# Optimization experiments

Measured on AMD Instinct MI355X. Metric: run time of the kernel, lower is better.

Reference implementation:

```python
import jax, jax.numpy as jnp
import numpy as np

LN_EPS = 1e-12
CHEB_K = 3
HIDDEN = 64


def _layernorm(x, w, b):
    m = jnp.mean(x, axis=-1, keepdims=True)
    v = jnp.mean((x - m) ** 2, axis=-1, keepdims=True)
    return (x - m) / jnp.sqrt(v + LN_EPS) * w + b


def _magcn(x, node_emb, time_emb, ln_w, ln_b, W_pool, b_pool):
    # x: [B,N,C]; node_emb: [N,D]; W_pool: [D,K,C,O]; b_pool: [D,O]
    e = _layernorm(node_emb + time_emb[None, :], ln_w, ln_b)  # dropout = identity (eval)
    supports = jax.nn.softmax(e @ e.T, axis=1)                # [N,N]
    N = e.shape[0]
    Ts = [jnp.eye(N, dtype=x.dtype), supports]
    for _ in range(2, CHEB_K):
        Ts.append(2.0 * supports @ Ts[-1] - Ts[-2])
    S = jnp.stack(Ts, axis=0)                                 # [K,N,N]
    weights = jnp.einsum('nd,dkio->nkio', e, W_pool)          # [N,K,C,O]
    bias = e @ b_pool                                         # [N,O]
    x_g = jnp.einsum('knm,bmc->bnkc', S, x)                   # [B,N,K,C]
    return jnp.einsum('bnki,nkio->bno', x_g, weights) + bias  # [B,N,O]


def setup_inputs() -> dict:
    key = jax.random.key(0)
    ks = jax.random.split(key, 10)
    B, N, C, H, D = 64, 1024, 64, HIDDEN, 16
    return {
        'x': jax.random.normal(ks[0], (B, N, C), jnp.float32),
        'norm_dis_matrix': jax.random.uniform(ks[1], (N, N), jnp.float32),
        'state': jax.random.normal(ks[2], (B, N, H), jnp.float32),
        'node_embeddings': jax.random.normal(ks[3], (N, D), jnp.float32),
        'node_flows': jax.random.normal(ks[4], (B, N), jnp.float32),
        'time_embeddings': jax.random.normal(ks[5], (D,), jnp.float32),
        'gate_W': jax.random.normal(ks[6], (D, CHEB_K, C + H, 2 * H), jnp.float32) * 0.1,
        'gate_b': jax.random.normal(ks[7], (D, 2 * H), jnp.float32) * 0.1,
        'gate_ln_w': jnp.ones((D,), jnp.float32),
        'gate_ln_b': jnp.zeros((D,), jnp.float32),
        'update_W': jax.random.normal(ks[8], (D, CHEB_K, C + H, H), jnp.float32) * 0.1,
        'update_b': jax.random.normal(ks[9], (D, H), jnp.float32) * 0.1,
        'update_ln_w': jnp.ones((D,), jnp.float32),
        'update_ln_b': jnp.zeros((D,), jnp.float32),
    }


def reference(x, norm_dis_matrix, state, node_embeddings, node_flows, time_embeddings,
              gate_W, gate_b, gate_ln_w, gate_ln_b,
              update_W, update_b, update_ln_w, update_ln_b):
    inp_state = jnp.concatenate([x, state], axis=-1)  # [B,N,C+H]
    z_r = jax.nn.sigmoid(_magcn(inp_state, node_embeddings, time_embeddings,
                                gate_ln_w, gate_ln_b, gate_W, gate_b))
    z, r = z_r[..., :HIDDEN], z_r[..., HIDDEN:]
    candidate = jnp.concatenate([x, z * state], axis=-1)
    hc = jnp.tanh(_magcn(candidate, node_embeddings, time_embeddings,
                         update_ln_w, update_ln_b, update_W, update_b))
    return r * state + (1.0 - r) * hc
```

## Files before the change

kernel.cpp:

```cpp
#include <hip/hip_runtime.h>
#include <hip/hip_bf16.h>

typedef __hip_bfloat16 bf16;
typedef __attribute__((ext_vector_type(8))) short bf16x8;
typedef __attribute__((ext_vector_type(4))) float f32x4;

constexpr int Bn = 64;
constexpr int Nn = 1024;
constexpr int Dd = 16;
constexpr int Cc = 64;
constexpr int Hh = 64;
constexpr int CI = 128;
constexpr int OG = 128;
constexpr int OU = 64;
constexpr int Jt = Bn * CI;

__device__ __forceinline__ float b2f(bf16 v) { return __bfloat162float(v); }
__device__ __forceinline__ float lo2f(unsigned u) { return __uint_as_float(u << 16); }
__device__ __forceinline__ float hi2f(unsigned u) { return __uint_as_float(u & 0xffff0000u); }
__device__ __forceinline__ float bfbits2f(unsigned short u) { return __uint_as_float(((unsigned)u) << 16); }
__device__ __forceinline__ unsigned short f2bfbits(float x) {
    bf16 h = __float2bfloat16(x);
    return *reinterpret_cast<unsigned short*>(&h);
}
__device__ __forceinline__ float rfl(float x) {
    return __int_as_float(__builtin_amdgcn_readfirstlane(__float_as_int(x)));
}

__device__ __forceinline__ float ldin(const void* p, size_t i, int flag) {
    return flag ? b2f(((const bf16*)p)[i]) : ((const float*)p)[i];
}

__device__ __forceinline__ void gload_lds16(const void* g, void* l) {
    __builtin_amdgcn_global_load_lds((const __attribute__((address_space(1))) void*)g,
                                     (__attribute__((address_space(3))) void*)l, 16, 0, 0);
}

__global__ void detect_kernel(const void* glnw, int* flag) {
    unsigned u = *(const unsigned*)glnw;
    *flag = (u == 0x3F800000u) ? 0 : 1;
}

__global__ void conv_f32(const void* __restrict__ src, float* __restrict__ dst,
                         int n, const int* __restrict__ flag) {
    const int f = *flag;
    for (int i = blockIdx.x * blockDim.x + threadIdx.x; i < n; i += gridDim.x * blockDim.x)
        dst[i] = ldin(src, i, f);
}

__global__ __launch_bounds__(256) void wtrans(const void* __restrict__ src, unsigned short* __restrict__ Wt,
                                              int O, int osh, const int* __restrict__ flag) {
    const int f = *flag;
    const int k0 = blockIdx.x * 64;
    const int d = blockIdx.y;
    __shared__ unsigned short tile[64][136];
    const int t = threadIdx.x;
    for (int idx = t; idx < 64 * O; idx += 256) {
        const int kk = idx >> osh, o = idx & (O - 1);
        tile[kk][o] = f2bfbits(ldin(src, ((size_t)d * 384 + k0 + kk) * O + o, f));
    }
    __syncthreads();
    for (int idx = t; idx < O * 64; idx += 256) {
        const int o = idx >> 6, kk = idx & 63;
        Wt[((size_t)d * O + o) * 384 + k0 + kk] = tile[kk][o];
    }
}

__global__ void ln_kernel(const void* __restrict__ nemb, const void* __restrict__ temb,
                          const void* __restrict__ wg, const void* __restrict__ bg,
                          const void* __restrict__ wu, const void* __restrict__ bu,
                          float* __restrict__ e_g, float* __restrict__ e_u,
                          const int* __restrict__ flag) {
    const int f = *flag;
    int t = blockIdx.x * blockDim.x + threadIdx.x;
    if (t >= 2 * Nn) return;
    int which = t >> 10;
    int n = t & (Nn - 1);
    float v[Dd];
    float mean = 0.f;
#pragma unroll
    for (int d = 0; d < Dd; d++) { v[d] = ldin(nemb, n * Dd + d, f) + ldin(temb, d, f); mean += v[d]; }
    mean *= (1.f / Dd);
    float var = 0.f;
#pragma unroll
    for (int d = 0; d < Dd; d++) { float c = v[d] - mean; var += c * c; }
    var *= (1.f / Dd);
    float inv = 1.f / sqrtf(var + 1e-12f);
    const void* w = which ? wu : wg;
    const void* bb = which ? bu : bg;
    float* e = which ? e_u : e_g;
#pragma unroll
    for (int d = 0; d < Dd; d++)
        e[n * Dd + d] = (v[d] - mean) * inv * ldin(w, d, f) + ldin(bb, d, f);
}

__global__ __launch_bounds__(256) void attn_kernel(const float* __restrict__ e, bf16* __restrict__ A) {
    __shared__ float en[Dd];
    __shared__ float logits[Nn];
    __shared__ float red[256];
    const int n = blockIdx.x, t = threadIdx.x;
    if (t < Dd) en[t] = e[n * Dd + t];
    __syncthreads();
    float lmax = -1e30f;
    for (int m = t; m < Nn; m += 256) {
        float s = 0.f;
#pragma unroll
        for (int d = 0; d < Dd; d++) s += en[d] * e[m * Dd + d];
        logits[m] = s;
        lmax = fmaxf(lmax, s);
    }
    red[t] = lmax; __syncthreads();
    for (int s = 128; s > 0; s >>= 1) { if (t < s) red[t] = fmaxf(red[t], red[t + s]); __syncthreads(); }
    const float M = red[0];
    __syncthreads();
    float lsum = 0.f;
    for (int m = t; m < Nn; m += 256) { float p = expf(logits[m] - M); logits[m] = p; lsum += p; }
    red[t] = lsum; __syncthreads();
    for (int s = 128; s > 0; s >>= 1) { if (t < s) red[t] += red[t + s]; __syncthreads(); }
    const float inv = 1.f / red[0];
    for (int m = t; m < Nn; m += 256) A[(size_t)n * Nn + m] = __float2bfloat16(logits[m] * inv);
}

__global__ __launch_bounds__(256) void build_xg0(const void* __restrict__ x, const void* __restrict__ oth,
                                                 bf16* __restrict__ xg0t, bf16* __restrict__ xg0s,
                                                 const int* __restrict__ flag, int oth_bf16) {
    const int f = *flag;
    const int b = blockIdx.x;
    const int n0 = blockIdx.y * 64;
    __shared__ bf16 tile[128][68];
    const int t = threadIdx.x;
#pragma unroll
    for (int idx = t; idx < 64 * 128; idx += 256) {
        const int n = idx >> 7, i = idx & 127;
        const size_t base = ((size_t)b << 10) + n0 + n;
        float v;
        if (i < Cc) v = ldin(x, base * Cc + i, f);
        else v = oth_bf16 ? b2f(((const bf16*)oth)[base * Hh + i - Cc])
                          : ldin(oth, base * Hh + i - Cc, f);
        tile[i][n] = __float2bfloat16(v);
        xg0s[base * CI + i] = tile[i][n];
    }
    __syncthreads();
#pragma unroll
    for (int idx = t; idx < 128 * 64; idx += 256) {
        const int i = idx >> 6, n = idx & 63;
        xg0t[((size_t)(b * CI + i) << 10) + n0 + n] = tile[i][n];
    }
}

__global__ __launch_bounds__(256) void agg_mfma(const bf16* __restrict__ Amat,
                                                const bf16* __restrict__ Xmat,
                                                const bf16* __restrict__ Sub,
                                                bf16* __restrict__ Ct,
                                                bf16* __restrict__ Cs,
                                                int cheb, int write_t) {
    __shared__ bf16 Atile[128 * 32];
    __shared__ bf16 Xtile[128 * 32];
    __shared__ unsigned short Ts[128 * 136];
    char* AtileC = (char*)Atile;
    char* XtileC = (char*)Xtile;

    const int t = threadIdx.x;
    const int lane = t & 63, w = t >> 6;
    const int j0 = blockIdx.x * 128;
    const int m0 = blockIdx.y * 128;
    const int wr = (w >> 1) * 64, wc = (w & 1) * 64;
    const int lr = lane & 15, lq = lane >> 4;

    f32x4 acc[4][4];
#pragma unroll
    for (int a = 0; a < 4; a++)
#pragma unroll
        for (int b = 0; b < 4; b++) acc[a][b] = (f32x4){0.f, 0.f, 0.f, 0.f};

    const int srow = w * 16 + (lane >> 2);
    const int scb = (lane & 3) * 16;

    for (int k0 = 0; k0 < Nn; k0 += 32) {
        __syncthreads();
#pragma unroll
        for (int p = 0; p < 2; p++) {
            const int row = p * 64 + srow;
            gload_lds16((const char*)Amat + (size_t)(m0 + row) * 2048 + k0 * 2 + scb,
                        AtileC + p * 4096 + w * 1024);
            gload_lds16((const char*)Xmat + (size_t)(j0 + row) * 2048 + k0 * 2 + scb,
                        XtileC + p * 4096 + w * 1024);
        }
        __syncthreads();
        bf16x8 af[4], xf[4];
#pragma unroll
        for (int fr = 0; fr < 4; fr++)
            af[fr] = *(const bf16x8*)(AtileC + (wr + fr * 16 + lr) * 64 + lq * 16);
#pragma unroll
        for (int fc = 0; fc < 4; fc++)
            xf[fc] = *(const bf16x8*)(XtileC + (wc + fc * 16 + lr) * 64 + lq * 16);
#pragma unroll
        for (int fr = 0; fr < 4; fr++)
#pragma unroll
            for (int fc = 0; fc < 4; fc++)
                acc[fr][fc] = __builtin_amdgcn_mfma_f32_16x16x32_bf16(af[fr], xf[fc], acc[fr][fc], 0, 0, 0);
    }

#pragma unroll
    for (int fr = 0; fr < 4; fr++) {
        const int ml = wr + fr * 16 + lq * 4;
        const int m = m0 + ml;
#pragma unroll
        for (int fc = 0; fc < 4; fc++) {
            const int i = wc + fc * 16 + lr;
            const int j = j0 + i;
            f32x4 v = acc[fr][fc];
            const size_t off = ((size_t)j << 10) + m;
            if (cheb) {
                const ushort4 s = *(const ushort4*)((const unsigned short*)Sub + off);
                v.x = 2.f * v.x - bfbits2f(s.x);
                v.y = 2.f * v.y - bfbits2f(s.y);
                v.z = 2.f * v.z - bfbits2f(s.z);
                v.w = 2.f * v.w - bfbits2f(s.w);
            }
            ushort4 o4;
            o4.x = f2bfbits(v.x); o4.y = f2bfbits(v.y); o4.z = f2bfbits(v.z); o4.w = f2bfbits(v.w);
            if (write_t) *(ushort4*)((unsigned short*)Ct + off) = o4;
            const unsigned short* pv = (const unsigned short*)&o4;
#pragma unroll
            for (int q = 0; q < 4; q++) Ts[(ml + q) * 136 + i] = pv[q];
        }
    }
    __syncthreads();
    const int b = j0 >> 7;
#pragma unroll
    for (int p = 0; p < 8; p++) {
        const int u = p * 256 + t;
        const int m = u >> 4, ig = (u & 15) * 8;
        const uint4 val = *(const uint4*)&Ts[m * 136 + ig];
        *(uint4*)((unsigned short*)Cs + (((size_t)b << 10) + m0 + m) * 128 + ig) = val;
    }
}

template<int G, int GATE>
__global__ __launch_bounds__(256, 2) void pernode_gemm(
    const bf16* __restrict__ x0, const bf16* __restrict__ x1, const bf16* __restrict__ x2,
    const float* __restrict__ e, const unsigned short* __restrict__ Wt,
    const float* __restrict__ bpool,
    const void* __restrict__ state, const float* __restrict__ r_in,
    bf16* __restrict__ zs, float* __restrict__ r_out, void* __restrict__ out,
    const int* __restrict__ flag)
{
    constexpr int OSTR = GATE ? 128 : 64;
    const int f = *flag;
    const int bx = blockIdx.x;
    const int grp = GATE ? (bx >> 1) : bx;
    const int obase = GATE ? ((bx & 1) << 6) : 0;
    const int n0 = grp * G;

    __shared__ bf16 Wl[8 * 64 * 32];
    __shared__ bf16 Xl[G * 64 * 32];
    char* WlC = (char*)Wl;
    char* XlC = (char*)Xl;

    const int t = threadIdx.x;
    const int lane = t & 63, w = t >> 6;
    const int lr = lane & 15, lq = lane >> 4;
    const int og = obase + w * 16 + lr;

    float en[G][16];
#pragma unroll
    for (int nl = 0; nl < G; nl++)
#pragma unroll
        for (int d = 0; d < 16; d++) en[nl][d] = rfl(e[(n0 + nl) * 16 + d]);

    f32x4 acc[G][4];
#pragma unroll
    for (int nl = 0; nl < G; nl++)
#pragma unroll
        for (int mt = 0; mt < 4; mt++) acc[nl][mt] = (f32x4){0.f, 0.f, 0.f, 0.f};

    const bf16* xs[3] = {x0, x1, x2};

#pragma unroll 1
    for (int ch = 0; ch < 3; ch++) {
        const bf16* Xsrc = xs[ch];
#pragma unroll 1
        for (int ks = 0; ks < 4; ks++) {
            float wacc[G][8];
#pragma unroll
            for (int nl = 0; nl < G; nl++)
#pragma unroll
                for (int j = 0; j < 8; j++) wacc[nl][j] = 0.f;

#pragma unroll
            for (int dh = 0; dh < 2; dh++) {
                __syncthreads();
#pragma unroll
                for (int p = 0; p < 8; p++) {
                    const int u = p * 256 + w * 64 + lane;
                    const int r = u >> 2, kg = u & 3;
                    const int d = r >> 6, ol = r & 63;
                    gload_lds16(Wt + ((size_t)((dh * 8 + d) * OSTR + obase + ol) * 384)
                                   + ch * 128 + ks * 32 + kg * 8,
                                WlC + u * 16);
                }
                if (dh == 0) {
#pragma unroll
                    for (int p = 0; p < G; p++) {
                        const int u = p * 256 + w * 64 + lane;
                        const int r = u >> 2, kg = u & 3;
                        const int nl = r >> 6, b = r & 63;
                        gload_lds16(Xsrc + (((size_t)b << 10) + n0 + nl) * 128 + ks * 32 + kg * 8,
                                    XlC + u * 16);
                    }
                }
                __syncthreads();
#pragma unroll
                for (int d = 0; d < 8; d++) {
                    const bf16x8 wv = *(const bf16x8*)(WlC + (d * 64 + w * 16 + lr) * 64 + lq * 16);
                    const unsigned* wu = (const unsigned*)&wv;
                    float v[8];
                    v[0] = lo2f(wu[0]); v[1] = hi2f(wu[0]);
                    v[2] = lo2f(wu[1]); v[3] = hi2f(wu[1]);
                    v[4] = lo2f(wu[2]); v[5] = hi2f(wu[2]);
                    v[6] = lo2f(wu[3]); v[7] = hi2f(wu[3]);
#pragma unroll
                    for (int nl = 0; nl < G; nl++) {
                        const float ed = en[nl][dh * 8 + d];
#pragma unroll
                        for (int j = 0; j < 8; j++) wacc[nl][j] += ed * v[j];
                    }
                }
            }
#pragma unroll
            for (int nl = 0; nl < G; nl++) {
                union U8 { bf16x8 v; unsigned short s[8]; } bh, bl;
#pragma unroll
                for (int j = 0; j < 8; j++) {
                    const unsigned short h = f2bfbits(wacc[nl][j]);
                    bh.s[j] = h;
                    bl.s[j] = f2bfbits(wacc[nl][j] - bfbits2f(h));
                }
#pragma unroll
                for (int mt = 0; mt < 4; mt++) {
                    const bf16x8 af = *(const bf16x8*)(XlC + (nl * 64 + mt * 16 + lr) * 64 + lq * 16);
                    acc[nl][mt] = __builtin_amdgcn_mfma_f32_16x16x32_bf16(af, bh.v, acc[nl][mt], 0, 0, 0);
                    acc[nl][mt] = __builtin_amdgcn_mfma_f32_16x16x32_bf16(af, bl.v, acc[nl][mt], 0, 0, 0);
                }
            }
        }
    }

    const int ol = og & 63;
#pragma unroll
    for (int nl = 0; nl < G; nl++) {
        const int n_ = n0 + nl;
        float bias = 0.f;
#pragma unroll
        for (int d = 0; d < 16; d++) bias += en[nl][d] * bpool[d * OSTR + og];
#pragma unroll
        for (int mt = 0; mt < 4; mt++) {
            const f32x4 a = acc[nl][mt];
#pragma unroll
            for (int q = 0; q < 4; q++) {
                const int b = mt * 16 + lq * 4 + q;
                const size_t idx = (((size_t)b << 10) + n_) * 64 + ol;
                const float v = a[q] + bias;
                if (GATE) {
                    const float sg = 1.f / (1.f + expf(-v));
                    if (obase == 0) {
                        const float st = ldin(state, idx, f);
                        zs[idx] = __float2bfloat16(sg * st);
                    } else {
                        r_out[idx] = sg;
                    }
                } else {
                    const float hc = tanhf(v);
                    const float r = r_in[idx];
                    const float st = ldin(state, idx, f);
                    const float o = r * st + (1.f - r) * hc;
                    if (f) ((bf16*)out)[idx] = __float2bfloat16(o);
                    else   ((float*)out)[idx] = o;
                }
            }
        }
    }
}

extern "C" void kernel_launch(void* const* d_in, const int* in_sizes, int n_in,
                              void* d_out, int out_size, void* d_ws, size_t ws_size,
                              hipStream_t stream) {
    const void* x     = d_in[0];
    const void* state = d_in[2];
    const void* nemb  = d_in[3];
    const void* temb  = d_in[5];
    const void* gW    = d_in[6];
    const void* gb    = d_in[7];
    const void* glnw  = d_in[8];
    const void* glnb  = d_in[9];
    const void* uW    = d_in[10];
    const void* ub    = d_in[11];
    const void* ulnw  = d_in[12];
    const void* ulnb  = d_in[13];

    constexpr int GW_N = Dd * 3 * CI * OG;
    constexpr int GB_N = Dd * OG;
    constexpr int UW_N = Dd * 3 * CI * OU;
    constexpr int UB_N = Dd * OU;

    char* base = (char*)d_ws;
    size_t off = 0;
    auto carve = [&](size_t bytes) { char* p = base + off; off += (bytes + 255) & ~(size_t)255; return p; };
    int*   flag = (int*)carve(4);
    unsigned short* gWt = (unsigned short*)carve(GW_N * 2);
    unsigned short* uWt = (unsigned short*)carve(UW_N * 2);
    float* gbf = (float*)carve(GB_N * 4);
    float* ubf = (float*)carve(UB_N * 4);
    float* e_g = (float*)carve(Nn * Dd * 4);
    float* e_u = (float*)carve(Nn * Dd * 4);
    bf16*  Abf  = (bf16*)carve((size_t)Nn * Nn * 2);
    bf16*  xg0t = (bf16*)carve((size_t)Jt * Nn * 2);
    bf16*  xg0s = (bf16*)carve((size_t)Jt * Nn * 2);
    bf16*  xg1t = (bf16*)carve((size_t)Jt * Nn * 2);
    bf16*  xg1s = (bf16*)carve((size_t)Jt * Nn * 2);
    bf16*  xg2s = (bf16*)carve((size_t)Jt * Nn * 2);
    bf16*  zs   = (bf16*)carve((size_t)Bn * Nn * Hh * 2);
    float* r_s  = (float*)carve((size_t)Bn * Nn * Hh * 4);
    if (ws_size < off) return;

    detect_kernel<<<1, 1, 0, stream>>>(glnw, flag);
    wtrans<<<dim3(6, 16), 256, 0, stream>>>(gW, gWt, OG, 7, flag);
    wtrans<<<dim3(6, 16), 256, 0, stream>>>(uW, uWt, OU, 6, flag);
    conv_f32<<<(GB_N + 255) / 256, 256, 0, stream>>>(gb, gbf, GB_N, flag);
    conv_f32<<<(UB_N + 255) / 256, 256, 0, stream>>>(ub, ubf, UB_N, flag);
    ln_kernel<<<8, 256, 0, stream>>>(nemb, temb, glnw, glnb, ulnw, ulnb, e_g, e_u, flag);

    attn_kernel<<<Nn, 256, 0, stream>>>(e_g, Abf);
    build_xg0<<<dim3(Bn, 16), 256, 0, stream>>>(x, state, xg0t, xg0s, flag, 0);
    agg_mfma<<<dim3(Jt / 128, Nn / 128), 256, 0, stream>>>(Abf, xg0t, nullptr, xg1t, xg1s, 0, 1);
    agg_mfma<<<dim3(Jt / 128, Nn / 128), 256, 0, stream>>>(Abf, xg1t, xg0t, xg1t, xg2s, 1, 0);
    pernode_gemm<4, 1><<<512, 256, 0, stream>>>(xg0s, xg1s, xg2s, e_g, gWt, gbf,
                                                state, nullptr, zs, r_s, nullptr, flag);

    attn_kernel<<<Nn, 256, 0, stream>>>(e_u, Abf);
    build_xg0<<<dim3(Bn, 16), 256, 0, stream>>>(x, zs, xg0t, xg0s, flag, 1);
    agg_mfma<<<dim3(Jt / 128, Nn / 128), 256, 0, stream>>>(Abf, xg0t, nullptr, xg1t, xg1s, 0, 1);
    agg_mfma<<<dim3(Jt / 128, Nn / 128), 256, 0, stream>>>(Abf, xg1t, xg0t, xg1t, xg2s, 1, 0);
    pernode_gemm<2, 0><<<512, 256, 0, stream>>>(xg0s, xg1s, xg2s, e_u, uWt, ubf,
                                                state, r_s, nullptr, nullptr, d_out, flag);
}
```

Baseline: 473.6 us.

## Double-buffer pernode_gemm loads with d-interleaved swizzled weight layout

Changes the transposed weight layout so that the eight embedding dims of a half are packed contiguously per (o,k), and adds an XOR swizzle to the LDS placement. pernode_gemm now flattens its phase loops into one loop that double-buffers weight and activation tiles, prefetching the next phase while computing the current one, with a single barrier per phase. The intent is to hide global-to-LDS latency and cut LDS bank conflicts. In exchange it doubles shared memory and drops the 2-blocks-per-SM launch bound, which may lower occupancy.

```diff
diff --git a/kernel.cpp b/kernel.cpp
--- a/kernel.cpp
+++ b/kernel.cpp
@@ -48,21 +48,27 @@
         dst[i] = ldin(src, i, f);
 }
 
-__global__ __launch_bounds__(256) void wtrans(const void* __restrict__ src, unsigned short* __restrict__ Wt,
-                                              int O, int osh, const int* __restrict__ flag) {
+__global__ __launch_bounds__(256) void wtrans2(const void* __restrict__ src, unsigned short* __restrict__ Wt,
+                                               int O, int osh, const int* __restrict__ flag) {
     const int f = *flag;
-    const int k0 = blockIdx.x * 64;
-    const int d = blockIdx.y;
-    __shared__ unsigned short tile[64][136];
+    const int k0 = blockIdx.x * 16;
+    const int dh = blockIdx.y;
+    __shared__ unsigned short tile[8 * 16 * 128];
     const int t = threadIdx.x;
-    for (int idx = t; idx < 64 * O; idx += 256) {
-        const int kk = idx >> osh, o = idx & (O - 1);
-        tile[kk][o] = f2bfbits(ldin(src, ((size_t)d * 384 + k0 + kk) * O + o, f));
+    const int total = 128 * O;
+    for (int idx = t; idx < total; idx += 256) {
+        const int o = idx & (O - 1);
+        const int r = idx >> osh;
+        const int kk = r & 15, dl = r >> 4;
+        tile[idx] = f2bfbits(ldin(src, ((size_t)(dh * 8 + dl) * 384 + k0 + kk) * O + o, f));
     }
     __syncthreads();
-    for (int idx = t; idx < O * 64; idx += 256) {
-        const int o = idx >> 6, kk = idx & 63;
-        Wt[((size_t)d * O + o) * 384 + k0 + kk] = tile[kk][o];
+    for (int u = t; u < 16 * O; u += 256) {
+        const int o = u >> 4, kk = u & 15;
+        unsigned short o8[8];
+#pragma unroll
+        for (int dl = 0; dl < 8; dl++) o8[dl] = tile[(dl * 16 + kk) * O + o];
+        *(uint4*)&Wt[((size_t)(dh * O + o) * 384 + k0 + kk) * 8] = *(const uint4*)o8;
     }
 }
 
@@ -238,7 +244,7 @@
 }
 
 template<int G, int GATE>
-__global__ __launch_bounds__(256, 2) void pernode_gemm(
+__global__ __launch_bounds__(256) void pernode_gemm(
     const bf16* __restrict__ x0, const bf16* __restrict__ x1, const bf16* __restrict__ x2,
     const float* __restrict__ e, const unsigned short* __restrict__ Wt,
     const float* __restrict__ bpool,
@@ -253,11 +259,8 @@
     const int obase = GATE ? ((bx & 1) << 6) : 0;
     const int n0 = grp * G;
 
-    __shared__ bf16 Wl[8 * 64 * 32];
-    __shared__ bf16 Xl[G * 64 * 32];
-    char* WlC = (char*)Wl;
-    char* XlC = (char*)Xl;
-
+    __shared__ bf16 Wb[2][16384];
+    __shared__ bf16 Xb[2][G * 2048];
     const int t = threadIdx.x;
     const int lane = t & 63, w = t >> 6;
     const int lr = lane & 15, lq = lane >> 4;
@@ -277,57 +280,71 @@
 
     const bf16* xs[3] = {x0, x1, x2};
 
+    auto issueW = [&](int wph, int buf) {
+        const int ch = wph >> 3, ks = (wph >> 1) & 3, dh = wph & 1;
+        char* dst = (char*)Wb[buf];
+#pragma unroll
+        for (int p = 0; p < 8; p++) {
+            const int u = p * 256 + t;
+            const int o = u >> 5;
+            const int kk = (u & 31) ^ (o & 7);
+            gload_lds16(Wt + ((size_t)(dh * OSTR + obase + o) * 384 + ch * 128 + ks * 32 + kk) * 8,
+                        dst + u * 16);
+        }
+    };
+    auto issueX = [&](int s, int buf) {
+        const int ch = s >> 2, ks = s & 3;
+        const bf16* Xsrc = xs[ch];
+        char* dst = (char*)Xb[buf];
+#pragma unroll
+        for (int p = 0; p < G; p++) {
+            const int u = p * 256 + t;
+            const int r = u >> 2, kg = u & 3;
+            const int nl = r >> 6, b = r & 63;
+            gload_lds16(Xsrc + (((size_t)b << 10) + n0 + nl) * 128 + ks * 32 + kg * 8,
+                        dst + u * 16);
+        }
+    };
+
+    issueW(0, 0);
+    issueX(0, 0);
+
+    float wacc[G][8];
 #pragma unroll 1
-    for (int ch = 0; ch < 3; ch++) {
-        const bf16* Xsrc = xs[ch];
-#pragma unroll 1
-        for (int ks = 0; ks < 4; ks++) {
-            float wacc[G][8];
+    for (int wph = 0; wph < 24; wph++) {
+        const int s = wph >> 1, dh = wph & 1;
+        __syncthreads();
+        if (wph + 1 < 24) issueW(wph + 1, (wph + 1) & 1);
+        if (dh == 0 && s + 1 < 12) issueX(s + 1, (s + 1) & 1);
+
+        if (dh == 0) {
 #pragma unroll
             for (int nl = 0; nl < G; nl++)
 #pragma unroll
                 for (int j = 0; j < 8; j++) wacc[nl][j] = 0.f;
-
-#pragma unroll
-            for (int dh = 0; dh < 2; dh++) {
-                __syncthreads();
-#pragma unroll
-                for (int p = 0; p < 8; p++) {
-                    const int u = p * 256 + w * 64 + lane;
-                    const int r = u >> 2, kg = u & 3;
-                    const int d = r >> 6, ol = r & 63;
-                    gload_lds16(Wt + ((size_t)((dh * 8 + d) * OSTR + obase + ol) * 384)
-                                   + ch * 128 + ks * 32 + kg * 8,
-                                WlC + u * 16);
-                }
-                if (dh == 0) {
-#pragma unroll
-                    for (int p = 0; p < G; p++) {
-                        const int u = p * 256 + w * 64 + lane;
-                        const int r = u >> 2, kg = u & 3;
-                        const int nl = r >> 6, b = r & 63;
-                        gload_lds16(Xsrc + (((size_t)b << 10) + n0 + nl) * 128 + ks * 32 + kg * 8,
-                                    XlC + u * 16);
-                    }
-                }
-                __syncthreads();
-#pragma unroll
-                for (int d = 0; d < 8; d++) {
-                    const bf16x8 wv = *(const bf16x8*)(WlC + (d * 64 + w * 16 + lr) * 64 + lq * 16);
-                    const unsigned* wu = (const unsigned*)&wv;
-                    float v[8];
-                    v[0] = lo2f(wu[0]); v[1] = hi2f(wu[0]);
-                    v[2] = lo2f(wu[1]); v[3] = hi2f(wu[1]);
-                    v[4] = lo2f(wu[2]); v[5] = hi2f(wu[2]);
-                    v[6] = lo2f(wu[3]); v[7] = hi2f(wu[3]);
-#pragma unroll
-                    for (int nl = 0; nl < G; nl++) {
-                        const float ed = en[nl][dh * 8 + d];
-#pragma unroll
-                        for (int j = 0; j < 8; j++) wacc[nl][j] += ed * v[j];
-                    }
-                }
+        }
+        const char* wsrc = (const char*)Wb[wph & 1];
+#pragma unroll
+        for (int j = 0; j < 8; j++) {
+            const int slot = (lq * 8 + j) ^ (lr & 7);
+            const bf16x8 wv = *(const bf16x8*)(wsrc + ((w * 16 + lr) * 32 + slot) * 16);
+            const unsigned* wu = (const unsigned*)&wv;
+            float v[8];
+            v[0] = lo2f(wu[0]); v[1] = hi2f(wu[0]);
+            v[2] = lo2f(wu[1]); v[3] = hi2f(wu[1]);
+            v[4] = lo2f(wu[2]); v[5] = hi2f(wu[2]);
+            v[6] = lo2f(wu[3]); v[7] = hi2f(wu[3]);
+#pragma unroll
+            for (int nl = 0; nl < G; nl++) {
+                float s8 = 0.f;
+#pragma unroll
+                for (int dl = 0; dl < 8; dl++) s8 += en[nl][dh * 8 + dl] * v[dl];
+                wacc[nl][j] += s8;
             }
+        }
+
+        if (dh == 1) {
+            const char* xsrc = (const char*)Xb[s & 1];
 #pragma unroll
             for (int nl = 0; nl < G; nl++) {
                 union U8 { bf16x8 v; unsigned short s[8]; } bh, bl;
@@ -339,7 +356,7 @@
                 }
 #pragma unroll
                 for (int mt = 0; mt < 4; mt++) {
-                    const bf16x8 af = *(const bf16x8*)(XlC + (nl * 64 + mt * 16 + lr) * 64 + lq * 16);
+                    const bf16x8 af = *(const bf16x8*)(xsrc + (nl * 64 + mt * 16 + lr) * 64 + lq * 16);
                     acc[nl][mt] = __builtin_amdgcn_mfma_f32_16x16x32_bf16(af, bh.v, acc[nl][mt], 0, 0, 0);
                     acc[nl][mt] = __builtin_amdgcn_mfma_f32_16x16x32_bf16(af, bl.v, acc[nl][mt], 0, 0, 0);
                 }
@@ -425,8 +442,8 @@
     if (ws_size < off) return;
 
     detect_kernel<<<1, 1, 0, stream>>>(glnw, flag);
-    wtrans<<<dim3(6, 16), 256, 0, stream>>>(gW, gWt, OG, 7, flag);
-    wtrans<<<dim3(6, 16), 256, 0, stream>>>(uW, uWt, OU, 6, flag);
+    wtrans2<<<dim3(24, 2), 256, 0, stream>>>(gW, gWt, OG, 7, flag);
+    wtrans2<<<dim3(24, 2), 256, 0, stream>>>(uW, uWt, OU, 6, flag);
     conv_f32<<<(GB_N + 255) / 256, 256, 0, stream>>>(gb, gbf, GB_N, flag);
     conv_f32<<<(UB_N + 255) / 256, 256, 0, stream>>>(ub, ubf, UB_N, flag);
     ln_kernel<<<8, 256, 0, stream>>>(nemb, temb, glnw, glnb, ulnw, ulnb, e_g, e_u, flag);
```

Result: slower. 862.1 us (+82.0%).

## Double-buffer per-node weight tiles in LDS to overlap loads with compute

Applied to the files above, without the earlier changes.

The per-node GEMM's nested channel/k-step/d-half loops are flattened into one 24-step loop. The weight-pool slice for the next step is now issued into a second LDS buffer while the current one is consumed, which halves the number of barriers per step and hides global-to-LDS latency behind the FMA and MFMA work. The launch-bounds minimum-blocks hint is dropped. The doubled weight LDS and the relaxed register budget may reduce how many blocks fit on each CU.

```diff
diff --git a/kernel.cpp b/kernel.cpp
--- a/kernel.cpp
+++ b/kernel.cpp
@@ -238,7 +238,7 @@
 }
 
 template<int G, int GATE>
-__global__ __launch_bounds__(256, 2) void pernode_gemm(
+__global__ __launch_bounds__(256) void pernode_gemm(
     const bf16* __restrict__ x0, const bf16* __restrict__ x1, const bf16* __restrict__ x2,
     const float* __restrict__ e, const unsigned short* __restrict__ Wt,
     const float* __restrict__ bpool,
@@ -253,9 +253,8 @@
     const int obase = GATE ? ((bx & 1) << 6) : 0;
     const int n0 = grp * G;
 
-    __shared__ bf16 Wl[8 * 64 * 32];
+    __shared__ bf16 Wb[2][8 * 64 * 32];
     __shared__ bf16 Xl[G * 64 * 32];
-    char* WlC = (char*)Wl;
     char* XlC = (char*)Xl;
 
     const int t = threadIdx.x;
@@ -277,55 +276,79 @@
 
     const bf16* xs[3] = {x0, x1, x2};
 
+    auto issueW = [&](int p) {
+        const int ch = p >> 3, ks = (p >> 1) & 3, dh = p & 1;
+        char* dst = (char*)Wb[p & 1];
+#pragma unroll
+        for (int pp = 0; pp < 8; pp++) {
+            const int u = pp * 256 + t;
+            const int r = u >> 2, kg = u & 3;
+            const int d = r >> 6, ol = r & 63;
+            gload_lds16(Wt + ((size_t)((dh * 8 + d) * OSTR + obase + ol) * 384)
+                           + ch * 128 + ks * 32 + kg * 8,
+                        dst + u * 16);
+        }
+    };
+    auto issueX = [&](int s) {
+        const int ch = s >> 2, ks = s & 3;
+        const bf16* Xsrc = xs[ch];
+#pragma unroll
+        for (int pp = 0; pp < G; pp++) {
+            const int u = pp * 256 + t;
+            const int r = u >> 2, kg = u & 3;
+            const int nl = r >> 6, b = r & 63;
+            gload_lds16(Xsrc + (((size_t)b << 10) + n0 + nl) * 128 + ks * 32 + kg * 8,
+                        XlC + u * 16);
+        }
+    };
+
+    issueW(0);
+
+    float wacc[G][8];
 #pragma unroll 1
-    for (int ch = 0; ch < 3; ch++) {
-        const bf16* Xsrc = xs[ch];
-#pragma unroll 1
-        for (int ks = 0; ks < 4; ks++) {
-            float wacc[G][8];
+    for (int p = 0; p < 24; p++) {
+        const int s = p >> 1, dh = p & 1;
+        __syncthreads();
+        if (dh == 0) issueX(s);
+        if (p + 1 < 24) issueW(p + 1);
+
+        const char* wsrc = (const char*)Wb[p & 1];
+        if (dh == 0) {
 #pragma unroll
             for (int nl = 0; nl < G; nl++)
 #pragma unroll
                 for (int j = 0; j < 8; j++) wacc[nl][j] = 0.f;
-
-#pragma unroll
-            for (int dh = 0; dh < 2; dh++) {
-                __syncthreads();
-#pragma unroll
-                for (int p = 0; p < 8; p++) {
-                    const int u = p * 256 + w * 64 + lane;
-                    const int r = u >> 2, kg = u & 3;
-                    const int d = r >> 6, ol = r & 63;
-                    gload_lds16(Wt + ((size_t)((dh * 8 + d) * OSTR + obase + ol) * 384)
-                                   + ch * 128 + ks * 32 + kg * 8,
-                                WlC + u * 16);
+#pragma unroll
+            for (int d = 0; d < 8; d++) {
+                const bf16x8 wv = *(const bf16x8*)(wsrc + (d * 64 + w * 16 + lr) * 64 + lq * 16);
+                const unsigned* wu = (const unsigned*)&wv;
+                float v[8];
+                v[0] = lo2f(wu[0]); v[1] = hi2f(wu[0]);
+                v[2] = lo2f(wu[1]); v[3] = hi2f(wu[1]);
+                v[4] = lo2f(wu[2]); v[5] = hi2f(wu[2]);
+                v[6] = lo2f(wu[3]); v[7] = hi2f(wu[3]);
+#pragma unroll
+                for (int nl = 0; nl < G; nl++) {
+                    const float ed = en[nl][d];
+#pragma unroll
+                    for (int j = 0; j < 8; j++) wacc[nl][j] += ed * v[j];
                 }
-                if (dh == 0) {
-#pragma unroll
-                    for (int p = 0; p < G; p++) {
-                        const int u = p * 256 + w * 64 + lane;
-                        const int r = u >> 2, kg = u & 3;
-                        const int nl = r >> 6, b = r & 63;
-                        gload_lds16(Xsrc + (((size_t)b << 10) + n0 + nl) * 128 + ks * 32 + kg * 8,
-                                    XlC + u * 16);
-                    }
-                }
-                __syncthreads();
-#pragma unroll
-                for (int d = 0; d < 8; d++) {
-                    const bf16x8 wv = *(const bf16x8*)(WlC + (d * 64 + w * 16 + lr) * 64 + lq * 16);
-                    const unsigned* wu = (const unsigned*)&wv;
-                    float v[8];
-                    v[0] = lo2f(wu[0]); v[1] = hi2f(wu[0]);
-                    v[2] = lo2f(wu[1]); v[3] = hi2f(wu[1]);
-                    v[4] = lo2f(wu[2]); v[5] = hi2f(wu[2]);
-                    v[6] = lo2f(wu[3]); v[7] = hi2f(wu[3]);
-#pragma unroll
-                    for (int nl = 0; nl < G; nl++) {
-                        const float ed = en[nl][dh * 8 + d];
-#pragma unroll
-                        for (int j = 0; j < 8; j++) wacc[nl][j] += ed * v[j];
-                    }
+            }
+        } else {
+#pragma unroll
+            for (int d = 0; d < 8; d++) {
+                const bf16x8 wv = *(const bf16x8*)(wsrc + (d * 64 + w * 16 + lr) * 64 + lq * 16);
+                const unsigned* wu = (const unsigned*)&wv;
+                float v[8];
+                v[0] = lo2f(wu[0]); v[1] = hi2f(wu[0]);
+                v[2] = lo2f(wu[1]); v[3] = hi2f(wu[1]);
+                v[4] = lo2f(wu[2]); v[5] = hi2f(wu[2]);
+                v[6] = lo2f(wu[3]); v[7] = hi2f(wu[3]);
+#pragma unroll
+                for (int nl = 0; nl < G; nl++) {
+                    const float ed = en[nl][8 + d];
+#pragma unroll
+                    for (int j = 0; j < 8; j++) wacc[nl][j] += ed * v[j];
                 }
             }
 #pragma unroll
```

Result: no change. 466.2 us (-1.6%).
